# Kernel optimization log

Measured on AMD Instinct MI355X. Metric: run time of the kernel, lower is better.

The kernel has to match this reference:

```python
import jax, jax.numpy as jnp
import numpy as np

N_HEADS = 16
D_HEAD = 64
N_ROTATE = 32
ROPE_BASE = 10000.0
MAX_LEN = 2048  # round_up_to_multiple_of_256(keep count); static for jit
BATCH, SEQ = 2, 4096


def setup_inputs() -> dict:
    key = jax.random.key(0)
    kq, kk, kv = jax.random.split(key, 3)
    q = jax.random.normal(kq, (BATCH, N_HEADS, MAX_LEN, D_HEAD), jnp.float32)
    k = jax.random.normal(kk, (BATCH, N_HEADS, SEQ, D_HEAD), jnp.float32)
    v = jax.random.normal(kv, (BATCH, N_HEADS, SEQ, D_HEAD), jnp.float32)
    # causal full mask [batch, seq, seq] and full position ids [batch, seq]
    mask_full = jnp.broadcast_to(jnp.tril(jnp.ones((SEQ, SEQ), bool)), (BATCH, SEQ, SEQ))
    pos_full = jnp.broadcast_to(jnp.arange(SEQ, dtype=jnp.int32), (BATCH, SEQ))
    # skip_mask: exactly MAX_LEN kept tokens per row (random positions)
    rng = np.random.default_rng(0)
    sm = np.zeros((BATCH, SEQ), dtype=bool)
    for i in range(BATCH):
        sm[i, rng.permutation(SEQ)[:MAX_LEN]] = True
    return {"q": q, "k": k, "v": v, "mask_full": mask_full,
            "pos_full": pos_full, "skip_mask": jnp.asarray(sm)}


def _rope_rotate(x, pos):
    # x: [b, h, L, n_rotate], pos: [b, L]
    half = N_ROTATE // 2
    inv_freq = 1.0 / (ROPE_BASE ** (jnp.arange(0, N_ROTATE, 2, dtype=jnp.float32) / N_ROTATE))
    freqs = pos.astype(jnp.float32)[..., None] * inv_freq          # [b, L, half]
    emb = jnp.concatenate([freqs, freqs], axis=-1)[:, None]        # [b, 1, L, n_rotate]
    cos, sin = jnp.cos(emb), jnp.sin(emb)
    x1, x2 = x[..., :half], x[..., half:]
    rot = jnp.concatenate([-x2, x1], axis=-1)                      # rotate_half
    return x * cos + rot * sin


def reference(q, k, v, mask_full, pos_full, skip_mask):
    b, S = skip_mask.shape
    lengths = skip_mask.sum(axis=1)
    # vectorized _trim_attention_mask: stable argsort compacts kept indices to the front
    order = jnp.argsort(jnp.where(skip_mask, 0, 1), axis=1, stable=True)
    idx = order[:, :MAX_LEN]                                       # [b, max_len]
    brow = jnp.arange(b)[:, None]
    mask_trim = mask_full[brow, idx]                               # [b, max_len, S]
    pos_trim = pos_full[brow, idx]                                 # [b, max_len]
    valid = jnp.arange(MAX_LEN)[None, :] < lengths[:, None]
    mask_trim = mask_trim & valid[..., None]
    pos_trim = jnp.where(valid, pos_trim, 0)

    # partial RoPE on first n_rotate channels
    rq = _rope_rotate(q[..., :N_ROTATE], pos_trim)
    rk = _rope_rotate(k[..., :N_ROTATE], pos_full)
    q = jnp.concatenate([rq, q[..., N_ROTATE:]], axis=-1)
    k = jnp.concatenate([rk, k[..., N_ROTATE:]], axis=-1)

    # masked SDPA (bool mask broadcast over heads)
    scale = 1.0 / jnp.sqrt(jnp.float32(D_HEAD))
    scores = jnp.einsum('bhqd,bhkd->bhqk', q, k) * scale
    scores = jnp.where(mask_trim[:, None], scores, jnp.finfo(scores.dtype).min)
    attn = jax.nn.softmax(scores, axis=-1)
    return jnp.einsum('bhqk,bhkd->bhqd', attn, v)
```

## Files before the change

### kernel.cpp

```cpp
#include <hip/hip_runtime.h>
#include <math.h>

#define BB 2
#define HH 16
#define QQ 2048
#define SS 4096
#define DD 64
#define NRH 16
#define NQT 32

typedef unsigned short u16;
typedef unsigned int   u32;
typedef short bhalf8 __attribute__((ext_vector_type(8)));
typedef float f32x4  __attribute__((ext_vector_type(4)));

typedef __attribute__((address_space(1))) const u32 gu32;
typedef __attribute__((address_space(3))) u32 lu32;

#if __has_builtin(__builtin_amdgcn_exp2f)
#define EXP2(x) __builtin_amdgcn_exp2f(x)
#else
#define EXP2(x) exp2f(x)
#endif

union Frag16 { uint4 u; bhalf8 v; u16 s[8]; uint2 d[2]; };

__device__ __forceinline__ u16 f2bf(float f) {
  union { float f; u32 u; } c; c.f = f;
  return (u16)((c.u + 0x7FFFu + ((c.u >> 16) & 1u)) >> 16);
}

__device__ __forceinline__ u32 cvt_pk_bf16(float lo, float hi) {
  u32 r;
  asm("v_cvt_pk_bf16_f32 %0, %1, %2" : "=v"(r) : "v"(lo), "v"(hi));
  return r;
}

__device__ __forceinline__ bhalf8 ldfrag(const u16* p) {
  Frag16 f; f.u = *reinterpret_cast<const uint4*>(p); return f.v;
}

__device__ __forceinline__ void rope32(float* x, int pos) {
  const float step = 0.8304820237218405f;
  const float fp = (float)pos;
#pragma unroll
  for (int i = 0; i < NRH; ++i) {
    float ang = fp * exp2f(-step * (float)i);
    float sv, cv;
    __sincosf(ang, &sv, &cv);
    float a = x[i], b = x[i + NRH];
    x[i]       = a * cv - b * sv;
    x[i + NRH] = b * cv + a * sv;
  }
}

__device__ __forceinline__ void prep_idx_body(const unsigned char* __restrict__ sm,
                                              int* __restrict__ idx, int b,
                                              int* wsum, int* modes) {
  const int tid = threadIdx.x;

  int c = 0;
  for (int i = 0; i < 32; ++i) c += (sm[tid * 32 + i] != 0) ? 1 : 0;
#pragma unroll
  for (int off = 32; off; off >>= 1) c += __shfl_down(c, off);
  if ((tid & 63) == 0) wsum[tid >> 6] = c;
  __syncthreads();
  if (tid == 0) *modes = (wsum[0] + wsum[1] + wsum[2] + wsum[3] > 3000) ? 1 : 0;
  __syncthreads();
  const bool byteMode = (*modes != 0);
  const u32* sm32 = (const u32*)sm;

  const int base = b * SS + tid * 16;
  u32 flags = 0;
  for (int i = 0; i < 16; ++i) {
    bool f = byteMode ? (sm[base + i] != 0) : (sm32[base + i] != 0);
    flags |= ((u32)(f ? 1 : 0)) << i;
  }
  int cnt = __popc(flags);
  int vv = cnt;
#pragma unroll
  for (int off = 1; off < 64; off <<= 1) {
    int t = __shfl_up(vv, off);
    if ((tid & 63) >= off) vv += t;
  }
  __syncthreads();
  if ((tid & 63) == 63) wsum[tid >> 6] = vv;
  __syncthreads();
  int add = 0;
  for (int w2 = 0; w2 < (tid >> 6); ++w2) add += wsum[w2];
  int p = vv - cnt + add;
  for (int i = 0; i < 16; ++i) {
    if (flags & (1u << i)) {
      if (p < QQ) idx[b * QQ + p] = tid * 16 + i;
      ++p;
    }
  }
}

__global__ void prep_idx_kernel(const unsigned char* __restrict__ sm,
                                int* __restrict__ idx) {
  __shared__ int wsum[4];
  __shared__ int modes;
  prep_idx_body(sm, idx, (int)blockIdx.x, wsum, &modes);
}

__global__ __launch_bounds__(256) void prep_fused_kernel(
    const float* __restrict__ k, const float* __restrict__ v,
    const unsigned char* __restrict__ skip,
    u16* __restrict__ kbf, u16* __restrict__ vt, int* __restrict__ idx) {
  __shared__ u16 tile[64][72];
  __shared__ int wsum[4];
  __shared__ int modes;
  if (blockIdx.x >= 2560) {
    prep_idx_body(skip, idx, (int)blockIdx.x - 2560, wsum, &modes);
  } else if (blockIdx.x < 512) {
    int r = blockIdx.x * 256 + threadIdx.x;
    int pos = r & (SS - 1);
    float x[64];
    const float4* src = (const float4*)(k + (size_t)r * DD);
#pragma unroll
    for (int i = 0; i < 16; ++i) {
      float4 t = src[i];
      x[4 * i] = t.x; x[4 * i + 1] = t.y; x[4 * i + 2] = t.z; x[4 * i + 3] = t.w;
    }
    rope32(x, pos);
    u16 tmp[64];
#pragma unroll
    for (int i = 0; i < 64; ++i) tmp[i] = f2bf(x[i]);
    uint4* dst = (uint4*)(kbf + (size_t)r * DD);
#pragma unroll
    for (int i = 0; i < 8; ++i) dst[i] = ((uint4*)tmp)[i];
  } else {
    int blk = (int)blockIdx.x - 512;
    int bh = blk >> 6;
    int jt = blk & 63;
    int t = threadIdx.x;
    int jl = t >> 2;
    int dc = (t & 3) * 16;
    const float4* src = (const float4*)(v + ((size_t)(bh * SS + jt * 64 + jl)) * DD + dc);
#pragma unroll
    for (int i = 0; i < 4; ++i) {
      float4 f = src[i];
      tile[jl][dc + 4 * i]     = f2bf(f.x);
      tile[jl][dc + 4 * i + 1] = f2bf(f.y);
      tile[jl][dc + 4 * i + 2] = f2bf(f.z);
      tile[jl][dc + 4 * i + 3] = f2bf(f.w);
    }
    __syncthreads();
    int d = t >> 2;
    int c = t & 3;
    u16 o[16];
#pragma unroll
    for (int m = 0; m < 16; ++m) {
      int p = c * 16 + m;
      int kp = (p & 32) | ((p & 4) << 2) | ((p >> 1) & 12) | (p & 3);
      o[m] = tile[kp][d];
    }
    uint4* dst = (uint4*)(vt + ((size_t)(bh * DD + d)) * SS + jt * 64 + c * 16);
    dst[0] = ((uint4*)o)[0];
    dst[1] = ((uint4*)o)[1];
  }
}

__device__ __forceinline__ void stage_tiles(const char* kb_bh, const char* vt_bh,
                                            u16* Kb, u16* Vb, int t0,
                                            int w, int srow, int schk) {
#pragma unroll
  for (int p2 = 0; p2 < 2; ++p2) {
    const int rr = w * 16 + p2 * 8 + srow;
    {
      const char* g = kb_bh + (size_t)(t0 + rr) * 128 + ((schk ^ (rr & 7)) * 16);
      lu32* l = (lu32*)((char*)Kb + (w * 16 + p2 * 8) * 128);
      __builtin_amdgcn_global_load_lds((gu32*)g, l, 16, 0, 0);
    }
    {
      const char* g = vt_bh + (size_t)rr * (SS * 2) + t0 * 2 + ((schk ^ (rr & 7)) * 16);
      lu32* l = (lu32*)((char*)Vb + (w * 16 + p2 * 8) * 128);
      __builtin_amdgcn_global_load_lds((gu32*)g, l, 16, 0, 0);
    }
  }
}

template <bool MASKED>
__device__ __forceinline__ void attn_tile(
    const u16* __restrict__ Kb, const u16* __restrict__ Vb,
    int t0, int grp, int col, int bnd,
    bhalf8 qa0, bhalf8 qa1,
    f32x4& acc0, f32x4& acc1, f32x4& acc2, f32x4& acc3,
    float& lsum) {
  const int swz = col & 7;
  f32x4 z = {0.f, 0.f, 0.f, 0.f};
  f32x4 s0 = z, s1 = z, s2 = z, s3 = z;
  {
    const u16* kr0 = Kb + (0 * 16 + col) * 64;
    const u16* kr1 = Kb + (1 * 16 + col) * 64;
    const u16* kr2 = Kb + (2 * 16 + col) * 64;
    const u16* kr3 = Kb + (3 * 16 + col) * 64;
    __builtin_amdgcn_s_setprio(1);
    bhalf8 a0 = ldfrag(kr0 + ((grp ^ swz) * 8));
    s0 = __builtin_amdgcn_mfma_f32_16x16x32_bf16(a0, qa0, s0, 0, 0, 0);
    bhalf8 b0 = ldfrag(kr0 + (((4 + grp) ^ swz) * 8));
    s0 = __builtin_amdgcn_mfma_f32_16x16x32_bf16(b0, qa1, s0, 0, 0, 0);
    bhalf8 a1 = ldfrag(kr1 + ((grp ^ swz) * 8));
    s1 = __builtin_amdgcn_mfma_f32_16x16x32_bf16(a1, qa0, s1, 0, 0, 0);
    bhalf8 b1 = ldfrag(kr1 + (((4 + grp) ^ swz) * 8));
    s1 = __builtin_amdgcn_mfma_f32_16x16x32_bf16(b1, qa1, s1, 0, 0, 0);
    bhalf8 a2 = ldfrag(kr2 + ((grp ^ swz) * 8));
    s2 = __builtin_amdgcn_mfma_f32_16x16x32_bf16(a2, qa0, s2, 0, 0, 0);
    bhalf8 b2 = ldfrag(kr2 + (((4 + grp) ^ swz) * 8));
    s2 = __builtin_amdgcn_mfma_f32_16x16x32_bf16(b2, qa1, s2, 0, 0, 0);
    bhalf8 a3 = ldfrag(kr3 + ((grp ^ swz) * 8));
    s3 = __builtin_amdgcn_mfma_f32_16x16x32_bf16(a3, qa0, s3, 0, 0, 0);
    bhalf8 b3 = ldfrag(kr3 + (((4 + grp) ^ swz) * 8));
    s3 = __builtin_amdgcn_mfma_f32_16x16x32_bf16(b3, qa1, s3, 0, 0, 0);
    __builtin_amdgcn_s_setprio(0);
  }

  uint2 w0, w1, w2, w3;
#define SM_C(SC, CB, W)                                                        \
  {                                                                            \
    float p0, p1, p2v, p3;                                                     \
    const int kb = t0 + (CB) + grp * 4;                                        \
    if (MASKED) {                                                              \
      p0  = (kb + 0 <= bnd) ? EXP2(SC[0] - 16.f) : 0.f;                        \
      p1  = (kb + 1 <= bnd) ? EXP2(SC[1] - 16.f) : 0.f;                        \
      p2v = (kb + 2 <= bnd) ? EXP2(SC[2] - 16.f) : 0.f;                        \
      p3  = (kb + 3 <= bnd) ? EXP2(SC[3] - 16.f) : 0.f;                        \
    } else {                                                                   \
      p0  = EXP2(SC[0] - 16.f);                                                \
      p1  = EXP2(SC[1] - 16.f);                                                \
      p2v = EXP2(SC[2] - 16.f);                                                \
      p3  = EXP2(SC[3] - 16.f);                                                \
    }                                                                          \
    lsum += (p0 + p1) + (p2v + p3);                                            \
    W.x = cvt_pk_bf16(p0, p1);                                                 \
    W.y = cvt_pk_bf16(p2v, p3);                                                \
  }
  SM_C(s0, 0,  w0)
  SM_C(s1, 16, w1)
  SM_C(s2, 32, w2)
  SM_C(s3, 48, w3)
#undef SM_C

  bhalf8 pv0, pv1;
  {
    Frag16 f0, f1;
    f0.d[0] = w0; f0.d[1] = w1;
    f1.d[0] = w2; f1.d[1] = w3;
    pv0 = f0.v; pv1 = f1.v;
  }

  {
    const u16* vr0 = Vb + (0  + col) * 64;
    const u16* vr1 = Vb + (16 + col) * 64;
    const u16* vr2 = Vb + (32 + col) * 64;
    const u16* vr3 = Vb + (48 + col) * 64;
    __builtin_amdgcn_s_setprio(1);
    bhalf8 x0 = ldfrag(vr0 + ((grp ^ swz) * 8));
    acc0 = __builtin_amdgcn_mfma_f32_16x16x32_bf16(x0, pv0, acc0, 0, 0, 0);
    bhalf8 y0 = ldfrag(vr0 + (((4 + grp) ^ swz) * 8));
    acc0 = __builtin_amdgcn_mfma_f32_16x16x32_bf16(y0, pv1, acc0, 0, 0, 0);
    bhalf8 x1 = ldfrag(vr1 + ((grp ^ swz) * 8));
    acc1 = __builtin_amdgcn_mfma_f32_16x16x32_bf16(x1, pv0, acc1, 0, 0, 0);
    bhalf8 y1 = ldfrag(vr1 + (((4 + grp) ^ swz) * 8));
    acc1 = __builtin_amdgcn_mfma_f32_16x16x32_bf16(y1, pv1, acc1, 0, 0, 0);
    bhalf8 x2 = ldfrag(vr2 + ((grp ^ swz) * 8));
    acc2 = __builtin_amdgcn_mfma_f32_16x16x32_bf16(x2, pv0, acc2, 0, 0, 0);
    bhalf8 y2 = ldfrag(vr2 + (((4 + grp) ^ swz) * 8));
    acc2 = __builtin_amdgcn_mfma_f32_16x16x32_bf16(y2, pv1, acc2, 0, 0, 0);
    bhalf8 x3 = ldfrag(vr3 + ((grp ^ swz) * 8));
    acc3 = __builtin_amdgcn_mfma_f32_16x16x32_bf16(x3, pv0, acc3, 0, 0, 0);
    bhalf8 y3 = ldfrag(vr3 + (((4 + grp) ^ swz) * 8));
    acc3 = __builtin_amdgcn_mfma_f32_16x16x32_bf16(y3, pv1, acc3, 0, 0, 0);
    __builtin_amdgcn_s_setprio(0);
  }
}

__global__ __launch_bounds__(256, 4) void attn_mfma_kernel(
    const float* __restrict__ qsrc, const u16* __restrict__ kbf,
    const u16* __restrict__ vt, const int* __restrict__ idx,
    float* __restrict__ out) {
  __shared__ u16 KbufA[64 * 64];
  __shared__ u16 VbufA[64 * 64];
  __shared__ u16 KbufB[64 * 64];
  __shared__ u16 VbufB[64 * 64];

  const int blk = (int)blockIdx.x;
  const int bh  = blk & 31;
  const int rank = blk >> 5;
  const int rmod = rank & 7;
  const int rdiv = rank >> 3;
  const int qt = (rdiv == 0) ? (31 - rmod)
               : (rdiv == 1) ? rmod
               : (rdiv == 2) ? (23 - rmod)
               : (8 + rmod);
  const int q0  = qt * 64;
  const int b   = bh >> 4;
  const int tid  = threadIdx.x;
  const int w    = tid >> 6;
  const int lane = tid & 63;
  const int grp  = lane >> 4;
  const int col  = lane & 15;

  const char* kb_bh = (const char*)(kbf + (size_t)bh * SS * DD);
  const char* vt_bh = (const char*)(vt + (size_t)bh * DD * SS);

  const int srow = lane >> 3;
  const int schk = lane & 7;

  const int* idxb = idx + b * QQ + q0;
  const int bnd = idxb[w * 16 + col];
  const int wave_minb = idxb[w * 16];
  const int wave_maxb = idxb[w * 16 + 15];
  const int maxbound  = idxb[63];
  const int ntiles = (maxbound >> 6) + 1;

  bhalf8 qa0, qa1;
  {
    const int qrow = q0 + w * 16 + col;
    const float* qr = qsrc + (size_t)(bh * QQ + qrow) * DD;
    const int lof = (grp & 1) * 8;
    float4 A0 = *(const float4*)(qr + lof);
    float4 A1 = *(const float4*)(qr + lof + 4);
    float4 B0 = *(const float4*)(qr + 16 + lof);
    float4 B1 = *(const float4*)(qr + 16 + lof + 4);
    float4 C0 = *(const float4*)(qr + 32 + grp * 8);
    float4 C1 = *(const float4*)(qr + 32 + grp * 8 + 4);
    float xlo[8] = {A0.x, A0.y, A0.z, A0.w, A1.x, A1.y, A1.z, A1.w};
    float xhi[8] = {B0.x, B0.y, B0.z, B0.w, B1.x, B1.y, B1.z, B1.w};
    float xq1[8] = {C0.x, C0.y, C0.z, C0.w, C1.x, C1.y, C1.z, C1.w};
    const float scq = 0.125f * 1.44269504088896f;
    const float fp = (float)bnd;
    Frag16 f0, f1;
#pragma unroll
    for (int j = 0; j < 8; ++j) {
      float ang = fp * exp2f(-0.8304820237218405f * (float)(lof + j));
      float sv, cv;
      __sincosf(ang, &sv, &cv);
      float val = (grp >= 2) ? (xhi[j] * cv + xlo[j] * sv)
                             : (xlo[j] * cv - xhi[j] * sv);
      f0.s[j] = f2bf(val * scq);
      f1.s[j] = f2bf(xq1[j] * scq);
    }
    qa0 = f0.v; qa1 = f1.v;
  }

  f32x4 z = {0.f, 0.f, 0.f, 0.f};
  f32x4 acc0 = z, acc1 = z, acc2 = z, acc3 = z;
  float lsum = 0.f;

#define ATTN_CALL(M, KB, VB, T0)                                               \
  attn_tile<M>(KB, VB, T0, grp, col, bnd, qa0, qa1, acc0, acc1, acc2, acc3, lsum)

  stage_tiles(kb_bh, vt_bh, KbufA, VbufA, 0, w, srow, schk);
  __syncthreads();

  for (int ti = 0; ti < ntiles; ti += 2) {
    const bool has1 = (ti + 1) < ntiles;
    if (has1) stage_tiles(kb_bh, vt_bh, KbufB, VbufB, (ti + 1) << 6, w, srow, schk);
    {
      const int t0 = ti << 6;
      if (t0 <= wave_maxb) {
        if (t0 + 63 <= wave_minb) ATTN_CALL(false, KbufA, VbufA, t0);
        else                      ATTN_CALL(true,  KbufA, VbufA, t0);
      }
    }
    __syncthreads();
    if (has1) {
      if (ti + 2 < ntiles)
        stage_tiles(kb_bh, vt_bh, KbufA, VbufA, (ti + 2) << 6, w, srow, schk);
      {
        const int t0 = (ti + 1) << 6;
        if (t0 <= wave_maxb) {
          if (t0 + 63 <= wave_minb) ATTN_CALL(false, KbufB, VbufB, t0);
          else                      ATTN_CALL(true,  KbufB, VbufB, t0);
        }
      }
      __syncthreads();
    }
  }
#undef ATTN_CALL

  lsum += __shfl_xor(lsum, 16);
  lsum += __shfl_xor(lsum, 32);
  const float inv = 1.f / lsum;
  float* ob = out + (size_t)(bh * QQ + q0 + w * 16 + col) * DD + grp * 4;
  {
    float4 t;
    t.x = acc0[0] * inv; t.y = acc0[1] * inv; t.z = acc0[2] * inv; t.w = acc0[3] * inv;
    *(float4*)(ob + 0) = t;
    t.x = acc1[0] * inv; t.y = acc1[1] * inv; t.z = acc1[2] * inv; t.w = acc1[3] * inv;
    *(float4*)(ob + 16) = t;
    t.x = acc2[0] * inv; t.y = acc2[1] * inv; t.z = acc2[2] * inv; t.w = acc2[3] * inv;
    *(float4*)(ob + 32) = t;
    t.x = acc3[0] * inv; t.y = acc3[1] * inv; t.z = acc3[2] * inv; t.w = acc3[3] * inv;
    *(float4*)(ob + 48) = t;
  }
}

__global__ __launch_bounds__(64) void attn_fb_kernel(const float* __restrict__ q,
                                                     const float* __restrict__ ksrc,
                                                     const float* __restrict__ v,
                                                     const int* __restrict__ idx,
                                                     float* __restrict__ out) {
  int t = (int)(gridDim.x - 1u - blockIdx.x);
  int sub = t >> 5;
  int bh = t & 31;
  int b = bh >> 4;
  int lane = threadIdx.x;
  int qi = sub * 64 + lane;
  const int bound = idx[b * QQ + qi];

  float qreg[64];
  {
    const float4* qp = (const float4*)(q + ((size_t)bh * QQ + qi) * DD);
#pragma unroll
    for (int i = 0; i < 16; ++i) {
      float4 t4 = qp[i];
      qreg[4 * i] = t4.x; qreg[4 * i + 1] = t4.y;
      qreg[4 * i + 2] = t4.z; qreg[4 * i + 3] = t4.w;
    }
  }
  rope32(qreg, bound);
#pragma unroll
  for (int i = 0; i < 64; ++i) qreg[i] *= 0.125f;

  const float* kbase = ksrc + (size_t)bh * SS * DD;
  const float* vbase = v + (size_t)bh * SS * DD;
  float acc[64];
#pragma unroll
  for (int i = 0; i < 64; ++i) acc[i] = 0.f;
  float mrun = -INFINITY, lrun = 0.f;

  for (int j = 0; j <= bound; ++j) {
    float ka[64];
    const float4* kp = (const float4*)(kbase + (size_t)j * DD);
#pragma unroll
    for (int i = 0; i < 16; ++i) {
      float4 t4 = kp[i];
      ka[4 * i] = t4.x; ka[4 * i + 1] = t4.y;
      ka[4 * i + 2] = t4.z; ka[4 * i + 3] = t4.w;
    }
    rope32(ka, j);
    float s0 = 0.f, s1 = 0.f, s2 = 0.f, s3 = 0.f;
#pragma unroll
    for (int i = 0; i < 16; ++i) {
      s0 = fmaf(qreg[4 * i], ka[4 * i], s0);
      s1 = fmaf(qreg[4 * i + 1], ka[4 * i + 1], s1);
      s2 = fmaf(qreg[4 * i + 2], ka[4 * i + 2], s2);
      s3 = fmaf(qreg[4 * i + 3], ka[4 * i + 3], s3);
    }
    float sc = (s0 + s1) + (s2 + s3);
    if (sc > mrun) {
      float alpha = __expf(mrun - sc);
      lrun *= alpha;
#pragma unroll
      for (int i = 0; i < 64; ++i) acc[i] *= alpha;
      mrun = sc;
    }
    float pw = __expf(sc - mrun);
    lrun += pw;
    const float4* vp = (const float4*)(vbase + (size_t)j * DD);
#pragma unroll
    for (int i = 0; i < 16; ++i) {
      float4 t4 = vp[i];
      acc[4 * i] = fmaf(pw, t4.x, acc[4 * i]);
      acc[4 * i + 1] = fmaf(pw, t4.y, acc[4 * i + 1]);
      acc[4 * i + 2] = fmaf(pw, t4.z, acc[4 * i + 2]);
      acc[4 * i + 3] = fmaf(pw, t4.w, acc[4 * i + 3]);
    }
  }
  float inv = 1.0f / lrun;
  float4* op = (float4*)(out + ((size_t)bh * QQ + qi) * DD);
#pragma unroll
  for (int i = 0; i < 16; ++i) {
    float4 t4;
    t4.x = acc[4 * i] * inv; t4.y = acc[4 * i + 1] * inv;
    t4.z = acc[4 * i + 2] * inv; t4.w = acc[4 * i + 3] * inv;
    op[i] = t4;
  }
}

extern "C" void kernel_launch(void* const* d_in, const int* in_sizes, int n_in,
                              void* d_out, int out_size, void* d_ws, size_t ws_size,
                              hipStream_t stream) {
  (void)in_sizes; (void)n_in; (void)out_size;
  const float* q = (const float*)d_in[0];
  const float* k = (const float*)d_in[1];
  const float* v = (const float*)d_in[2];
  const unsigned char* skip = (const unsigned char*)d_in[5];
  float* out = (float*)d_out;

  char* base = (char*)d_ws;
  int* idx = (int*)base;
  const size_t kbytes = (size_t)BB * HH * SS * DD * 2;
  u16* kbf = (u16*)(base + 16384);
  u16* vtb = (u16*)(base + 16384 + kbytes);
  const size_t need = 16384 + 2 * kbytes;

  if (ws_size >= need) {
    prep_fused_kernel<<<512 + BB * HH * 64 + BB, 256, 0, stream>>>(k, v, skip,
                                                                   kbf, vtb, idx);
    attn_mfma_kernel<<<NQT * 32, 256, 0, stream>>>(q, kbf, vtb, idx, out);
  } else {
    prep_idx_kernel<<<2, 256, 0, stream>>>(skip, idx);
    attn_fb_kernel<<<1024, 64, 0, stream>>>(q, k, v, idx, out);
  }
}
```

Measured before the change: 283.1 us.

## Load V fragments directly from global memory instead of staging through LDS

Drops the V tile staging into shared memory. Each wave now loads its V^T fragments straight from global memory at the start of each tile, so the loads overlap with the QK MFMAs and softmax. This halves LDS use and the async LDS copy traffic, which may allow more occupancy. The cost is redundant global/L2 reads of V by all four waves in a block, plus strided per-lane 16-byte loads whose latency may not be fully hidden.

```diff
diff --git a/kernel.cpp b/kernel.cpp
--- a/kernel.cpp
+++ b/kernel.cpp
@@ -162,33 +162,39 @@
   }
 }
 
-__device__ __forceinline__ void stage_tiles(const char* kb_bh, const char* vt_bh,
-                                            u16* Kb, u16* Vb, int t0,
-                                            int w, int srow, int schk) {
+__device__ __forceinline__ void stage_k(const char* kb_bh, u16* Kb, int t0,
+                                        int w, int srow, int schk) {
 #pragma unroll
   for (int p2 = 0; p2 < 2; ++p2) {
     const int rr = w * 16 + p2 * 8 + srow;
-    {
-      const char* g = kb_bh + (size_t)(t0 + rr) * 128 + ((schk ^ (rr & 7)) * 16);
-      lu32* l = (lu32*)((char*)Kb + (w * 16 + p2 * 8) * 128);
-      __builtin_amdgcn_global_load_lds((gu32*)g, l, 16, 0, 0);
-    }
-    {
-      const char* g = vt_bh + (size_t)rr * (SS * 2) + t0 * 2 + ((schk ^ (rr & 7)) * 16);
-      lu32* l = (lu32*)((char*)Vb + (w * 16 + p2 * 8) * 128);
-      __builtin_amdgcn_global_load_lds((gu32*)g, l, 16, 0, 0);
-    }
+    const char* g = kb_bh + (size_t)(t0 + rr) * 128 + ((schk ^ (rr & 7)) * 16);
+    lu32* l = (lu32*)((char*)Kb + (w * 16 + p2 * 8) * 128);
+    __builtin_amdgcn_global_load_lds((gu32*)g, l, 16, 0, 0);
   }
 }
 
 template <bool MASKED>
 __device__ __forceinline__ void attn_tile(
-    const u16* __restrict__ Kb, const u16* __restrict__ Vb,
+    const u16* __restrict__ Kb, const char* __restrict__ vt_bh,
     int t0, int grp, int col, int bnd,
     bhalf8 qa0, bhalf8 qa1,
     f32x4& acc0, f32x4& acc1, f32x4& acc2, f32x4& acc3,
     float& lsum) {
   const int swz = col & 7;
+
+  const char* vr0 = vt_bh + (size_t)(0  + col) * (SS * 2) + (size_t)t0 * 2;
+  const char* vr1 = vt_bh + (size_t)(16 + col) * (SS * 2) + (size_t)t0 * 2;
+  const char* vr2 = vt_bh + (size_t)(32 + col) * (SS * 2) + (size_t)t0 * 2;
+  const char* vr3 = vt_bh + (size_t)(48 + col) * (SS * 2) + (size_t)t0 * 2;
+  bhalf8 x0 = ldfrag((const u16*)(vr0 + grp * 16));
+  bhalf8 y0 = ldfrag((const u16*)(vr0 + (4 + grp) * 16));
+  bhalf8 x1 = ldfrag((const u16*)(vr1 + grp * 16));
+  bhalf8 y1 = ldfrag((const u16*)(vr1 + (4 + grp) * 16));
+  bhalf8 x2 = ldfrag((const u16*)(vr2 + grp * 16));
+  bhalf8 y2 = ldfrag((const u16*)(vr2 + (4 + grp) * 16));
+  bhalf8 x3 = ldfrag((const u16*)(vr3 + grp * 16));
+  bhalf8 y3 = ldfrag((const u16*)(vr3 + (4 + grp) * 16));
+
   f32x4 z = {0.f, 0.f, 0.f, 0.f};
   f32x4 s0 = z, s1 = z, s2 = z, s3 = z;
   {
@@ -251,26 +257,14 @@
   }
 
   {
-    const u16* vr0 = Vb + (0  + col) * 64;
-    const u16* vr1 = Vb + (16 + col) * 64;
-    const u16* vr2 = Vb + (32 + col) * 64;
-    const u16* vr3 = Vb + (48 + col) * 64;
     __builtin_amdgcn_s_setprio(1);
-    bhalf8 x0 = ldfrag(vr0 + ((grp ^ swz) * 8));
     acc0 = __builtin_amdgcn_mfma_f32_16x16x32_bf16(x0, pv0, acc0, 0, 0, 0);
-    bhalf8 y0 = ldfrag(vr0 + (((4 + grp) ^ swz) * 8));
     acc0 = __builtin_amdgcn_mfma_f32_16x16x32_bf16(y0, pv1, acc0, 0, 0, 0);
-    bhalf8 x1 = ldfrag(vr1 + ((grp ^ swz) * 8));
     acc1 = __builtin_amdgcn_mfma_f32_16x16x32_bf16(x1, pv0, acc1, 0, 0, 0);
-    bhalf8 y1 = ldfrag(vr1 + (((4 + grp) ^ swz) * 8));
     acc1 = __builtin_amdgcn_mfma_f32_16x16x32_bf16(y1, pv1, acc1, 0, 0, 0);
-    bhalf8 x2 = ldfrag(vr2 + ((grp ^ swz) * 8));
     acc2 = __builtin_amdgcn_mfma_f32_16x16x32_bf16(x2, pv0, acc2, 0, 0, 0);
-    bhalf8 y2 = ldfrag(vr2 + (((4 + grp) ^ swz) * 8));
     acc2 = __builtin_amdgcn_mfma_f32_16x16x32_bf16(y2, pv1, acc2, 0, 0, 0);
-    bhalf8 x3 = ldfrag(vr3 + ((grp ^ swz) * 8));
     acc3 = __builtin_amdgcn_mfma_f32_16x16x32_bf16(x3, pv0, acc3, 0, 0, 0);
-    bhalf8 y3 = ldfrag(vr3 + (((4 + grp) ^ swz) * 8));
     acc3 = __builtin_amdgcn_mfma_f32_16x16x32_bf16(y3, pv1, acc3, 0, 0, 0);
     __builtin_amdgcn_s_setprio(0);
   }
@@ -281,9 +275,7 @@
     const u16* __restrict__ vt, const int* __restrict__ idx,
     float* __restrict__ out) {
   __shared__ u16 KbufA[64 * 64];
-  __shared__ u16 VbufA[64 * 64];
   __shared__ u16 KbufB[64 * 64];
-  __shared__ u16 VbufB[64 * 64];
 
   const int blk = (int)blockIdx.x;
   const int bh  = blk & 31;
@@ -349,31 +341,31 @@
   f32x4 acc0 = z, acc1 = z, acc2 = z, acc3 = z;
   float lsum = 0.f;
 
-#define ATTN_CALL(M, KB, VB, T0)                                               \
-  attn_tile<M>(KB, VB, T0, grp, col, bnd, qa0, qa1, acc0, acc1, acc2, acc3, lsum)
-
-  stage_tiles(kb_bh, vt_bh, KbufA, VbufA, 0, w, srow, schk);
+#define ATTN_CALL(M, KB, T0)                                                   \
+  attn_tile<M>(KB, vt_bh, T0, grp, col, bnd, qa0, qa1, acc0, acc1, acc2, acc3, lsum)
+
+  stage_k(kb_bh, KbufA, 0, w, srow, schk);
   __syncthreads();
 
   for (int ti = 0; ti < ntiles; ti += 2) {
     const bool has1 = (ti + 1) < ntiles;
-    if (has1) stage_tiles(kb_bh, vt_bh, KbufB, VbufB, (ti + 1) << 6, w, srow, schk);
+    if (has1) stage_k(kb_bh, KbufB, (ti + 1) << 6, w, srow, schk);
     {
       const int t0 = ti << 6;
       if (t0 <= wave_maxb) {
-        if (t0 + 63 <= wave_minb) ATTN_CALL(false, KbufA, VbufA, t0);
-        else                      ATTN_CALL(true,  KbufA, VbufA, t0);
+        if (t0 + 63 <= wave_minb) ATTN_CALL(false, KbufA, t0);
+        else                      ATTN_CALL(true,  KbufA, t0);
       }
     }
     __syncthreads();
     if (has1) {
       if (ti + 2 < ntiles)
-        stage_tiles(kb_bh, vt_bh, KbufA, VbufA, (ti + 2) << 6, w, srow, schk);
+        stage_k(kb_bh, KbufA, (ti + 2) << 6, w, srow, schk);
       {
         const int t0 = (ti + 1) << 6;
         if (t0 <= wave_maxb) {
-          if (t0 + 63 <= wave_minb) ATTN_CALL(false, KbufB, VbufB, t0);
-          else                      ATTN_CALL(true,  KbufB, VbufB, t0);
+          if (t0 + 63 <= wave_minb) ATTN_CALL(false, KbufB, t0);
+          else                      ATTN_CALL(true,  KbufB, t0);
         }
       }
       __syncthreads();
```

After: 368.6 us. 30.2% more time.
